# Optimization experiments

Measured on AMD Instinct MI355X. Metric: run time of the kernel, lower is better.

## Reference

```python
import jax, jax.numpy as jnp
import numpy as np

H = 8
DH = 64  # attention_head_size
HID = 512
NEG = -90000000000.0

def _lin(x, w, b):
    return x @ w + b

def _tfs(x):  # [N, HID] -> [H, N, DH]
    n = x.shape[0]
    return x.reshape(n, H, DH).transpose(1, 0, 2)

def _cross(q, ck, v, cv, mask, dw, db):
    # q: [H,N,DH], ck/cv: [H,M,DH], v: [H,N,DH], mask: [N,M]
    s = jnp.einsum('hnd,hmd->hnm', q, ck)
    s = s * mask[None, :, :] / jnp.sqrt(jnp.asarray(DH, s.dtype))
    s = jnp.where(s == 0.0, NEG, s)  # faithful zero->-inf hack
    p = jax.nn.softmax(s, axis=-1)
    ctx = v + jnp.einsum('hnm,hmd->hnd', p, cv)  # residual add of raw value
    n = ctx.shape[1]
    ctx = ctx.transpose(1, 0, 2).reshape(n, H * DH)
    return _lin(ctx, dw, db)

def setup_inputs() -> dict:
    key = jax.random.key(0)
    ks = jax.random.split(key, 24)
    N1, N2, D1 = 4096, 4096, 300
    d = {}
    d['h_head'] = jax.random.normal(ks[0], (N1, D1), jnp.float32)
    d['h_tail'] = jax.random.normal(ks[1], (N2, HID), jnp.float32)
    d['batch_head'] = jnp.sort(jax.random.randint(ks[2], (N1,), 0, 64))
    d['batch_tail'] = jnp.sort(jax.random.randint(ks[3], (N2,), 0, 64))
    def w(k, i, o):
        return jax.random.normal(k, (i, o), jnp.float32) / np.sqrt(i)
    d['map_w'] = w(ks[4], D1, HID); d['map_b'] = jnp.zeros((HID,), jnp.float32)
    names = ['q1', 'k1', 'v1', 'q2', 'k2', 'v2', 'd1', 'd2']
    for i, nm in enumerate(names):
        d[nm + '_w'] = w(ks[5 + i], HID, HID)
        d[nm + '_b'] = jnp.zeros((HID,), jnp.float32)
    return d

def reference(h_head, h_tail, batch_head, batch_tail,
              map_w, map_b,
              q1_w, q1_b, k1_w, k1_b, v1_w, v1_b,
              q2_w, q2_b, k2_w, k2_b, v2_w, v2_b,
              d1_w, d1_b, d2_w, d2_b):
    hh = _lin(h_head, map_w, map_b)  # n_dim1 != n_dim2 -> map
    q_h = _tfs(_lin(hh, q1_w, q1_b))
    k_h = _tfs(_lin(hh, k1_w, k1_b))
    v_h = _tfs(_lin(hh, v1_w, v1_b))
    q_t = _tfs(_lin(h_tail, q2_w, q2_b))
    k_t = _tfs(_lin(h_tail, k2_w, k2_b))
    v_t = _tfs(_lin(h_tail, v2_w, v2_b))
    mask = (batch_head[:, None] == batch_tail[None, :]).astype(jnp.float32)
    out_head = _cross(q_h, k_t, v_h, v_t, mask, d1_w, d1_b)
    out_tail = _cross(q_t, k_h, v_t, v_h, mask.T, d2_w, d2_b)
    return (out_head, out_tail)
```

## Files before the change

kernel.cpp:

```cpp
#include <hip/hip_runtime.h>
#include <hip/hip_bf16.h>
#include <math.h>


typedef __bf16 bf16x8 __attribute__((ext_vector_type(8)));
typedef __bf16 bf16x4 __attribute__((ext_vector_type(4)));
typedef float  f32x4  __attribute__((ext_vector_type(4)));

#define HID 512
#define NTOK 4096

#define AS1(p) ((const __attribute__((address_space(1))) void*)(p))
#define AS3(p) ((__attribute__((address_space(3))) void*)(p))

__device__ __forceinline__ void fold_tile(
    const float* __restrict__ Wf,
    const float* __restrict__ Mw,
    const float* __restrict__ Mb,
    __bf16* __restrict__ F,
    int bx, int by, char* SMEM)
{
    __bf16* As = (__bf16*)SMEM;
    __bf16* Bs = (__bf16*)(SMEM + 8192);

    const int tid  = threadIdx.x;
    const int wave = tid >> 6;
    const int lane = tid & 63;
    const int quad = lane >> 4;
    const int l16  = lane & 15;
    const int wy   = wave >> 1;
    const int wx   = wave & 1;
    const int rowBase = by * 128;
    const int colBase = bx * 128;

    const int s_row = tid >> 2;
    const int s_gc  = (tid & 3) ^ ((s_row >> 1) & 3);
    const int a_j4 = (tid & 7) * 4;
    const int a_n4 = (tid >> 3) * 4;

    float aR[16];
    float4 b0lo, b0hi, b1lo, b1hi;

    auto loadA = [&](int j0) {
        #pragma unroll
        for (int u = 0; u < 4; ++u)
            *(float4*)&aR[u * 4] =
                *(const float4*)&Wf[(size_t)(j0 + a_j4 + u) * 512 + rowBase + a_n4];
    };
    auto loadRow = [&](int k, int jc, float4& lo, float4& hi) {
        if (k < 300) {
            lo = *(const float4*)&Mw[(size_t)k * 512 + jc];
            hi = *(const float4*)&Mw[(size_t)k * 512 + jc + 4];
        } else if (k == 300) {
            lo = *(const float4*)&Mb[jc];
            hi = *(const float4*)&Mb[jc + 4];
        } else {
            lo = float4{0.f, 0.f, 0.f, 0.f};
            hi = float4{0.f, 0.f, 0.f, 0.f};
        }
    };
    auto loadB = [&](int j0) {
        const int jc = j0 + s_gc * 8;
        loadRow(colBase + s_row,      jc, b0lo, b0hi);
        loadRow(colBase + 64 + s_row, jc, b1lo, b1hi);
    };

    f32x4 acc[4][4] = {};

    loadA(0);
    loadB(0);

    for (int i = 0; i < 16; ++i) {
        __syncthreads();
        #pragma unroll
        for (int v = 0; v < 4; ++v) {
            const int r = a_n4 + v;
            const int p = (a_j4 >> 3) ^ ((r >> 1) & 3);
            bf16x4 w;
            w[0] = (__bf16)aR[0 * 4 + v];
            w[1] = (__bf16)aR[1 * 4 + v];
            w[2] = (__bf16)aR[2 * 4 + v];
            w[3] = (__bf16)aR[3 * 4 + v];
            *(bf16x4*)&As[r * 32 + p * 8 + (a_j4 & 7)] = w;
        }
        {
            bf16x8 v0, v1;
            v0[0]=(__bf16)b0lo.x; v0[1]=(__bf16)b0lo.y; v0[2]=(__bf16)b0lo.z; v0[3]=(__bf16)b0lo.w;
            v0[4]=(__bf16)b0hi.x; v0[5]=(__bf16)b0hi.y; v0[6]=(__bf16)b0hi.z; v0[7]=(__bf16)b0hi.w;
            v1[0]=(__bf16)b1lo.x; v1[1]=(__bf16)b1lo.y; v1[2]=(__bf16)b1lo.z; v1[3]=(__bf16)b1lo.w;
            v1[4]=(__bf16)b1hi.x; v1[5]=(__bf16)b1hi.y; v1[6]=(__bf16)b1hi.z; v1[7]=(__bf16)b1hi.w;
            *(bf16x8*)&Bs[tid * 8]        = v0;
            *(bf16x8*)&Bs[2048 + tid * 8] = v1;
        }
        if (i + 1 < 16) { loadA((i + 1) * 32); loadB((i + 1) * 32); }
        __syncthreads();

        bf16x8 ar[4], br[4];
        #pragma unroll
        for (int ii = 0; ii < 4; ++ii) {
            const int ra = wy * 64 + ii * 16 + l16;
            ar[ii] = *(const bf16x8*)&As[ra * 32 + ((quad ^ ((ra >> 1) & 3)) << 3)];
        }
        #pragma unroll
        for (int jj = 0; jj < 4; ++jj) {
            const int rb = wx * 64 + jj * 16 + l16;
            br[jj] = *(const bf16x8*)&Bs[rb * 32 + ((quad ^ ((rb >> 1) & 3)) << 3)];
        }
        #pragma unroll
        for (int ii = 0; ii < 4; ++ii)
            #pragma unroll
            for (int jj = 0; jj < 4; ++jj)
                acc[ii][jj] = __builtin_amdgcn_mfma_f32_16x16x32_bf16(ar[ii], br[jj], acc[ii][jj], 0, 0, 0);
    }

    #pragma unroll
    for (int jj = 0; jj < 4; ++jj) {
        int col = colBase + wx * 64 + jj * 16 + l16;
        if (col < 320) {
            #pragma unroll
            for (int ii = 0; ii < 4; ++ii) {
                #pragma unroll
                for (int r = 0; r < 4; ++r) {
                    int row = rowBase + wy * 64 + ii * 16 + quad * 4 + r;
                    F[(size_t)row * 320 + col] = (__bf16)acc[ii][jj][r];
                }
            }
        }
    }
}

struct PrepArgs {
    const float* h_head; const float* h_tail;
    const int* bh; const int* bt;
    const float* map_w; const float* map_b;
    const float* qkvw[3];
    const float* tsrc[5]; __bf16* tdst[5];
    __bf16* hh_bf; __bf16* ht_bf;
    __bf16* F[3];
    int* ranges;
};

__global__ __launch_bounds__(256) void fused_prep(PrepArgs pa) {
    const int q = blockIdx.x, z = blockIdx.z, tid = threadIdx.x;
    __shared__ __align__(16) char SMEM[16384];

    if (z == 0) {
        if (q == 0 && tid < 128) {
            int b = tid & 63;
            const int* arr = (tid < 64) ? pa.bh : pa.bt;
            int base = (tid < 64) ? 0 : 128;
            int lo = 0, hi = NTOK;
            while (lo < hi) { int mid = (lo + hi) >> 1; if (arr[mid] < b) lo = mid + 1; else hi = mid; }
            int start = lo;
            lo = 0; hi = NTOK;
            while (lo < hi) { int mid = (lo + hi) >> 1; if (arr[mid] <= b) lo = mid + 1; else hi = mid; }
            pa.ranges[base + b] = start;
            pa.ranges[base + 64 + b] = lo;
        }
        for (int idx = tid; idx < 8 * 40; idx += 256) {
            int r   = q * 8 + idx / 40;
            int col = (idx % 40) * 8;
            bf16x8 v;
            if (col + 8 <= 300) {
                float4 f0 = *(const float4*)&pa.h_head[(size_t)r * 300 + col];
                float4 f1 = *(const float4*)&pa.h_head[(size_t)r * 300 + col + 4];
                v[0]=(__bf16)f0.x; v[1]=(__bf16)f0.y; v[2]=(__bf16)f0.z; v[3]=(__bf16)f0.w;
                v[4]=(__bf16)f1.x; v[5]=(__bf16)f1.y; v[6]=(__bf16)f1.z; v[7]=(__bf16)f1.w;
            } else if (col < 300) {
                float4 f0 = *(const float4*)&pa.h_head[(size_t)r * 300 + col];
                v[0]=(__bf16)f0.x; v[1]=(__bf16)f0.y; v[2]=(__bf16)f0.z; v[3]=(__bf16)f0.w;
                v[4]=(__bf16)1.0f;
                v[5]=(__bf16)0.f; v[6]=(__bf16)0.f; v[7]=(__bf16)0.f;
            } else {
                #pragma unroll
                for (int j = 0; j < 8; ++j) v[j] = (__bf16)0.f;
            }
            *(bf16x8*)&pa.hh_bf[(size_t)r * 320 + col] = v;
        }
    } else if (z == 1) {
        for (int idx = tid; idx < 8 * 64; idx += 256) {
            int r   = q * 8 + (idx >> 6);
            int col = (idx & 63) * 8;
            float4 f0 = *(const float4*)&pa.h_tail[(size_t)r * 512 + col];
            float4 f1 = *(const float4*)&pa.h_tail[(size_t)r * 512 + col + 4];
            bf16x8 v;
            v[0]=(__bf16)f0.x; v[1]=(__bf16)f0.y; v[2]=(__bf16)f0.z; v[3]=(__bf16)f0.w;
            v[4]=(__bf16)f1.x; v[5]=(__bf16)f1.y; v[6]=(__bf16)f1.z; v[7]=(__bf16)f1.w;
            *(bf16x8*)&pa.ht_bf[(size_t)r * 512 + col] = v;
        }
    } else if (z == 2) {
        if (q >= 36) return;
        const int f = q / 12, t = q % 12;
        fold_tile(pa.qkvw[f], pa.map_w, pa.map_b, pa.F[f], t % 3, t / 3, SMEM);
    } else {
        if (q >= 64) return;
        typedef __bf16 trow[72];
        trow* T = (trow*)SMEM;
        const int jz = z - 3;
        const float* src = pa.tsrc[jz];
        __bf16* dst = pa.tdst[jz];
        const int tk = (q >> 3) * 64;
        const int tn = (q & 7) * 64;
        const int r0 = tid >> 4;
        const int c0 = (tid & 15) * 4;
        #pragma unroll
        for (int i = 0; i < 4; ++i) {
            float4 v = *(const float4*)&src[(size_t)(tk + r0 + i * 16) * 512 + tn + c0];
            T[r0 + i * 16][c0 + 0] = (__bf16)v.x;
            T[r0 + i * 16][c0 + 1] = (__bf16)v.y;
            T[r0 + i * 16][c0 + 2] = (__bf16)v.z;
            T[r0 + i * 16][c0 + 3] = (__bf16)v.w;
        }
        __syncthreads();
        const int n  = tid >> 2;
        const int kk = (tid & 3) * 16;
        bf16x8 o0, o1;
        #pragma unroll
        for (int j = 0; j < 8; ++j) { o0[j] = T[kk + j][n]; o1[j] = T[kk + 8 + j][n]; }
        __bf16* dp = dst + (size_t)(tn + n) * 512 + tk + kk;
        *(bf16x8*)dp       = o0;
        *(bf16x8*)(dp + 8) = o1;
    }
}

struct GemmJobs {
    const __bf16* A[6];
    const __bf16* W[6];
    const float*  bias[6];
    void*         C[6];
    int           Kp[6];
};

template <typename TC>
__global__ __launch_bounds__(256) void gemm128(GemmJobs jobs) {
    __shared__ __align__(16) __bf16 As[2][4096];
    __shared__ __align__(16) __bf16 Bs[2][4096];

    const int z = blockIdx.z;
    const __bf16* A    = jobs.A[z];
    const __bf16* W    = jobs.W[z];
    const float*  bias = jobs.bias[z];
    TC*           C    = (TC*)jobs.C[z];
    const int     Kp   = jobs.Kp[z];

    const int tid  = threadIdx.x;
    const int wave = tid >> 6;
    const int lane = tid & 63;
    const int quad = lane >> 4;
    const int l16  = lane & 15;
    const int wy   = wave >> 1;
    const int wx   = wave & 1;
    const int rowBase = blockIdx.y * 128;
    const int colBase = blockIdx.x * 128;

    const int s_row = tid >> 2;
    const int s_kc  = ((tid & 3) ^ ((s_row >> 1) & 3)) * 8;

    const __bf16* gA = A + (size_t)(rowBase + s_row) * Kp + s_kc;
    const __bf16* gB = W + (size_t)(colBase + s_row) * Kp + s_kc;
    const int waveOff = wave * 512;

    f32x4 acc[4][4] = {};
    const int nk = Kp >> 5;

    __builtin_amdgcn_global_load_lds(AS1(gA),                   AS3(&As[0][waveOff]),        16, 0, 0);
    __builtin_amdgcn_global_load_lds(AS1(gA + (size_t)64 * Kp), AS3(&As[0][2048 + waveOff]), 16, 0, 0);
    __builtin_amdgcn_global_load_lds(AS1(gB),                   AS3(&Bs[0][waveOff]),        16, 0, 0);
    __builtin_amdgcn_global_load_lds(AS1(gB + (size_t)64 * Kp), AS3(&Bs[0][2048 + waveOff]), 16, 0, 0);

    for (int i = 0; i < nk; ++i) {
        const int cur = i & 1;
        __syncthreads();

        if (i + 1 < nk) {
            const int kt = (i + 1) * 32;
            const int nx = cur ^ 1;
            __builtin_amdgcn_global_load_lds(AS1(gA + kt),                   AS3(&As[nx][waveOff]),        16, 0, 0);
            __builtin_amdgcn_global_load_lds(AS1(gA + kt + (size_t)64 * Kp), AS3(&As[nx][2048 + waveOff]), 16, 0, 0);
            __builtin_amdgcn_global_load_lds(AS1(gB + kt),                   AS3(&Bs[nx][waveOff]),        16, 0, 0);
            __builtin_amdgcn_global_load_lds(AS1(gB + kt + (size_t)64 * Kp), AS3(&Bs[nx][2048 + waveOff]), 16, 0, 0);
        }

        bf16x8 ar[4], br[4];
        #pragma unroll
        for (int ii = 0; ii < 4; ++ii) {
            const int ra = wy * 64 + ii * 16 + l16;
            ar[ii] = *(const bf16x8*)&As[cur][ra * 32 + ((quad ^ ((ra >> 1) & 3)) << 3)];
        }
        #pragma unroll
        for (int jj = 0; jj < 4; ++jj) {
            const int rb = wx * 64 + jj * 16 + l16;
            br[jj] = *(const bf16x8*)&Bs[cur][rb * 32 + ((quad ^ ((rb >> 1) & 3)) << 3)];
        }
        #pragma unroll
        for (int ii = 0; ii < 4; ++ii)
            #pragma unroll
            for (int jj = 0; jj < 4; ++jj)
                acc[ii][jj] = __builtin_amdgcn_mfma_f32_16x16x32_bf16(ar[ii], br[jj], acc[ii][jj], 0, 0, 0);
    }

    #pragma unroll
    for (int jj = 0; jj < 4; ++jj) {
        int col = colBase + wx * 64 + jj * 16 + l16;
        float bv = bias[col];
        #pragma unroll
        for (int ii = 0; ii < 4; ++ii) {
            #pragma unroll
            for (int r = 0; r < 4; ++r) {
                int row = rowBase + wy * 64 + ii * 16 + quad * 4 + r;
                C[(size_t)row * HID + col] = (TC)(acc[ii][jj][r] + bv);
            }
        }
    }
}

__global__ __launch_bounds__(256) void attn_mfma(
    const __bf16* __restrict__ Q0, const __bf16* __restrict__ K0,
    const __bf16* __restrict__ Vr0, const __bf16* __restrict__ Vc0,
    const __bf16* __restrict__ Q1, const __bf16* __restrict__ K1,
    const __bf16* __restrict__ Vr1, const __bf16* __restrict__ Vc1,
    const int* __restrict__ ranges,
    __bf16* __restrict__ O0, __bf16* __restrict__ O1,
    int Nq, int Nk)
{
    __shared__ __align__(16) __bf16 Qs[64][72];
    __shared__ __align__(16) __bf16 Ks[64][72];
    __shared__ __align__(16) __bf16 Vt[64][72];
    __shared__ __align__(16) __bf16 Ps[64][72];

    const int z = blockIdx.z;
    const __bf16* Q    = z ? Q1 : Q0;
    const __bf16* Kg   = z ? K1 : K0;
    const __bf16* Vres = z ? Vr1 : Vr0;
    const __bf16* Vctx = z ? Vc1 : Vc0;
    __bf16* Out        = z ? O1 : O0;
    const int* qstart  = z ? ranges + 128 : ranges;
    const int* qend    = z ? ranges + 192 : ranges + 64;
    const int* kstart  = z ? ranges       : ranges + 128;
    const int* kend    = z ? ranges + 64  : ranges + 192;

    const int h = blockIdx.x, b = blockIdx.y;
    const int qs = qstart[b], qe = qend[b];
    const int ts = kstart[b], te = kend[b];
    const int nq = qe - qs, nk = te - ts;
    if (nq <= 0) return;

    const int tid  = threadIdx.x;
    const int wave = tid >> 6;
    const int lane = tid & 63;
    const int quad = lane >> 4;
    const int l16  = lane & 15;
    const int srow = tid >> 2;
    const int scol = (tid & 3) * 16;

    if (nk <= 0) {
        float* meanv = (float*)Qs;
        if (tid < 64) {
            float s = 0.f;
            for (int m = 0; m < Nk; ++m)
                s += (float)Vctx[(size_t)m * HID + h * 64 + tid];
            meanv[tid] = s / (float)Nk;
        }
        __syncthreads();
        int d = tid & 63;
        for (int r = qs + (tid >> 6); r < qe; r += 4) {
            size_t off = (size_t)r * HID + h * 64 + d;
            Out[off] = (__bf16)((float)Vres[off] + meanv[d]);
        }
        return;
    }

    for (int qc = 0; qc < nq; qc += 64) {
        __syncthreads();
        {
            int qg = min(qs + qc + srow, Nq - 1);
            const __bf16* src = Q + (size_t)qg * HID + h * 64 + scol;
            *(bf16x8*)&Qs[srow][scol]     = *(const bf16x8*)src;
            *(bf16x8*)&Qs[srow][scol + 8] = *(const bf16x8*)(src + 8);
        }
        __syncthreads();
        bf16x8 aq0 = *(const bf16x8*)&Qs[wave * 16 + l16][quad * 8];
        bf16x8 aq1 = *(const bf16x8*)&Qs[wave * 16 + l16][32 + quad * 8];

        f32x4 O[4] = {};
        float Mx[4], L[4];
        #pragma unroll
        for (int r = 0; r < 4; ++r) { Mx[r] = -__builtin_inff(); L[r] = 0.f; }

        for (int kc = 0; kc < nk; kc += 64) {
            __syncthreads();
            {
                int kg = min(ts + kc + srow, Nk - 1);
                const __bf16* ksrc = Kg + (size_t)kg * HID + h * 64 + scol;
                *(bf16x8*)&Ks[srow][scol]     = *(const bf16x8*)ksrc;
                *(bf16x8*)&Ks[srow][scol + 8] = *(const bf16x8*)(ksrc + 8);
                const __bf16* vsrc = Vctx + (size_t)kg * HID + h * 64 + scol;
                bf16x8 v0 = *(const bf16x8*)vsrc;
                bf16x8 v1 = *(const bf16x8*)(vsrc + 8);
                #pragma unroll
                for (int j = 0; j < 8; ++j) {
                    Vt[scol + j][srow]     = v0[j];
                    Vt[scol + 8 + j][srow] = v1[j];
                }
            }
            __syncthreads();

            f32x4 S[4] = {};
            #pragma unroll
            for (int c = 0; c < 4; ++c) {
                bf16x8 bk0 = *(const bf16x8*)&Ks[c * 16 + l16][quad * 8];
                bf16x8 bk1 = *(const bf16x8*)&Ks[c * 16 + l16][32 + quad * 8];
                S[c] = __builtin_amdgcn_mfma_f32_16x16x32_bf16(aq0, bk0, S[c], 0, 0, 0);
                S[c] = __builtin_amdgcn_mfma_f32_16x16x32_bf16(aq1, bk1, S[c], 0, 0, 0);
            }

            #pragma unroll
            for (int c = 0; c < 4; ++c) {
                bool valid = (ts + kc + c * 16 + l16) < te;
                #pragma unroll
                for (int r = 0; r < 4; ++r)
                    S[c][r] = valid ? S[c][r] * 0.125f : -__builtin_inff();
            }

            float cm[4], ps[4], alpha[4];
            #pragma unroll
            for (int r = 0; r < 4; ++r) {
                float v = fmaxf(fmaxf(S[0][r], S[1][r]), fmaxf(S[2][r], S[3][r]));
                v = fmaxf(v, __shfl_xor(v, 1, 64));
                v = fmaxf(v, __shfl_xor(v, 2, 64));
                v = fmaxf(v, __shfl_xor(v, 4, 64));
                v = fmaxf(v, __shfl_xor(v, 8, 64));
                cm[r] = v;
            }
            #pragma unroll
            for (int r = 0; r < 4; ++r) {
                float nM = fmaxf(Mx[r], cm[r]);
                alpha[r] = __expf(Mx[r] - nM);
                Mx[r] = nM;
                ps[r] = 0.f;
            }
            #pragma unroll
            for (int c = 0; c < 4; ++c)
                #pragma unroll
                for (int r = 0; r < 4; ++r) {
                    float p = __expf(S[c][r] - Mx[r]);
                    S[c][r] = p;
                    ps[r] += p;
                }
            #pragma unroll
            for (int r = 0; r < 4; ++r) {
                float v = ps[r];
                v += __shfl_xor(v, 1, 64);
                v += __shfl_xor(v, 2, 64);
                v += __shfl_xor(v, 4, 64);
                v += __shfl_xor(v, 8, 64);
                L[r] = L[r] * alpha[r] + v;
            }
            #pragma unroll
            for (int c = 0; c < 4; ++c)
                #pragma unroll
                for (int r = 0; r < 4; ++r)
                    O[c][r] *= alpha[r];

            #pragma unroll
            for (int c = 0; c < 4; ++c)
                #pragma unroll
                for (int r = 0; r < 4; ++r)
                    Ps[wave * 16 + quad * 4 + r][c * 16 + l16] = (__bf16)S[c][r];
            __syncthreads();

            bf16x8 ap0 = *(const bf16x8*)&Ps[wave * 16 + l16][quad * 8];
            bf16x8 ap1 = *(const bf16x8*)&Ps[wave * 16 + l16][32 + quad * 8];
            #pragma unroll
            for (int c = 0; c < 4; ++c) {
                bf16x8 bv0 = *(const bf16x8*)&Vt[c * 16 + l16][quad * 8];
                bf16x8 bv1 = *(const bf16x8*)&Vt[c * 16 + l16][32 + quad * 8];
                O[c] = __builtin_amdgcn_mfma_f32_16x16x32_bf16(ap0, bv0, O[c], 0, 0, 0);
                O[c] = __builtin_amdgcn_mfma_f32_16x16x32_bf16(ap1, bv1, O[c], 0, 0, 0);
            }
        }

        #pragma unroll
        for (int c = 0; c < 4; ++c) {
            int d = h * 64 + c * 16 + l16;
            #pragma unroll
            for (int r = 0; r < 4; ++r) {
                int qrow = qs + qc + wave * 16 + quad * 4 + r;
                if (qrow < qe) {
                    size_t off = (size_t)qrow * HID + d;
                    Out[off] = (__bf16)((float)Vres[off] + O[c][r] / L[r]);
                }
            }
        }
    }
}

extern "C" void kernel_launch(void* const* d_in, const int* in_sizes, int n_in,
                              void* d_out, int out_size, void* d_ws, size_t ws_size,
                              hipStream_t stream) {
    (void)in_sizes; (void)n_in; (void)out_size; (void)ws_size;

    const float* h_head = (const float*)d_in[0];
    const float* h_tail = (const float*)d_in[1];
    const int* batch_head = (const int*)d_in[2];
    const int* batch_tail = (const int*)d_in[3];
    const float* map_w = (const float*)d_in[4];
    const float* map_b = (const float*)d_in[5];
    const float* q1_w = (const float*)d_in[6];
    const float* q1_b = (const float*)d_in[7];
    const float* k1_w = (const float*)d_in[8];
    const float* k1_b = (const float*)d_in[9];
    const float* v1_w = (const float*)d_in[10];
    const float* v1_b = (const float*)d_in[11];
    const float* q2_w = (const float*)d_in[12];
    const float* q2_b = (const float*)d_in[13];
    const float* k2_w = (const float*)d_in[14];
    const float* k2_b = (const float*)d_in[15];
    const float* v2_w = (const float*)d_in[16];
    const float* v2_b = (const float*)d_in[17];
    const float* d1_w = (const float*)d_in[18];
    const float* d1_b = (const float*)d_in[19];
    const float* d2_w = (const float*)d_in[20];
    const float* d2_b = (const float*)d_in[21];

    float* out = (float*)d_out;

    const size_t SZ = (size_t)NTOK * HID;
    char* ws = (char*)d_ws;
    int* ranges   = (int*)ws;
    __bf16* hh_bf = (__bf16*)(ws + 1024);
    __bf16* ht_bf = hh_bf + (size_t)NTOK * 320;
    __bf16* q2T  = ht_bf + SZ;
    __bf16* k2T  = q2T + 512 * 512;
    __bf16* v2T  = k2T + 512 * 512;
    __bf16* d1T  = v2T + 512 * 512;
    __bf16* d2T  = d1T + 512 * 512;
    __bf16* FqT  = d2T + 512 * 512;
    __bf16* FkT  = FqT + 512 * 320;
    __bf16* FvT  = FkT + 512 * 320;
    __bf16* qh   = FvT + 512 * 320;
    __bf16* kh   = qh  + SZ;
    __bf16* vh   = kh  + SZ;
    __bf16* qt   = vh  + SZ;
    __bf16* kt   = qt  + SZ;
    __bf16* vt   = kt  + SZ;
    __bf16* ctxh = vt  + SZ;
    __bf16* ctxt = ctxh + SZ;

    PrepArgs pa;
    pa.h_head = h_head; pa.h_tail = h_tail;
    pa.bh = batch_head; pa.bt = batch_tail;
    pa.map_w = map_w; pa.map_b = map_b;
    pa.qkvw[0] = q1_w; pa.qkvw[1] = k1_w; pa.qkvw[2] = v1_w;
    const float* wsrc[5] = {q2_w, k2_w, v2_w, d1_w, d2_w};
    __bf16* wdst[5] = {q2T, k2T, v2T, d1T, d2T};
    for (int i = 0; i < 5; ++i) { pa.tsrc[i] = wsrc[i]; pa.tdst[i] = wdst[i]; }
    pa.hh_bf = hh_bf; pa.ht_bf = ht_bf;
    pa.F[0] = FqT; pa.F[1] = FkT; pa.F[2] = FvT;
    pa.ranges = ranges;
    fused_prep<<<dim3(512, 1, 8), dim3(256), 0, stream>>>(pa);

    {
        GemmJobs j;
        j.A[0] = hh_bf; j.W[0] = FqT; j.bias[0] = q1_b; j.C[0] = qh; j.Kp[0] = 320;
        j.A[1] = hh_bf; j.W[1] = FkT; j.bias[1] = k1_b; j.C[1] = kh; j.Kp[1] = 320;
        j.A[2] = hh_bf; j.W[2] = FvT; j.bias[2] = v1_b; j.C[2] = vh; j.Kp[2] = 320;
        j.A[3] = ht_bf; j.W[3] = q2T; j.bias[3] = q2_b; j.C[3] = qt; j.Kp[3] = 512;
        j.A[4] = ht_bf; j.W[4] = k2T; j.bias[4] = k2_b; j.C[4] = kt; j.Kp[4] = 512;
        j.A[5] = ht_bf; j.W[5] = v2T; j.bias[5] = v2_b; j.C[5] = vt; j.Kp[5] = 512;
        gemm128<__bf16><<<dim3(4, 32, 6), dim3(256), 0, stream>>>(j);
    }

    attn_mfma<<<dim3(8, 64, 2), dim3(256), 0, stream>>>(
        qh, kt, vh, vt,
        qt, kh, vt, vh,
        ranges, ctxh, ctxt, NTOK, NTOK);

    {
        GemmJobs j;
        j.A[0] = ctxh; j.W[0] = d1T; j.bias[0] = d1_b; j.C[0] = out;      j.Kp[0] = 512;
        j.A[1] = ctxt; j.W[1] = d2T; j.bias[1] = d2_b; j.C[1] = out + SZ; j.Kp[1] = 512;
        j.A[2] = ctxt; j.W[2] = d2T; j.bias[2] = d2_b; j.C[2] = out + SZ; j.Kp[2] = 512;
        j.A[3] = ctxt; j.W[3] = d2T; j.bias[3] = d2_b; j.C[3] = out + SZ; j.Kp[3] = 512;
        j.A[4] = ctxt; j.W[4] = d2T; j.bias[4] = d2_b; j.C[4] = out + SZ; j.Kp[4] = 512;
        j.A[5] = ctxt; j.W[5] = d2T; j.bias[5] = d2_b; j.C[5] = out + SZ; j.Kp[5] = 512;
        gemm128<float><<<dim3(4, 32, 2), dim3(256), 0, stream>>>(j);
    }
}
```

Before: 184.0 us.

## Read fp32 weights directly in GEMM, drop weight transpose prep stage

```diff
diff --git a/kernel.cpp b/kernel.cpp
--- a/kernel.cpp
+++ b/kernel.cpp
@@ -9,9 +9,6 @@
 
 #define HID 512
 #define NTOK 4096
-
-#define AS1(p) ((const __attribute__((address_space(1))) void*)(p))
-#define AS3(p) ((__attribute__((address_space(3))) void*)(p))
 
 __device__ __forceinline__ void fold_tile(
     const float* __restrict__ Wf,
@@ -134,7 +131,6 @@
     const int* bh; const int* bt;
     const float* map_w; const float* map_b;
     const float* qkvw[3];
-    const float* tsrc[5]; __bf16* tdst[5];
     __bf16* hh_bf; __bf16* ht_bf;
     __bf16* F[3];
     int* ranges;
@@ -188,60 +184,36 @@
             v[4]=(__bf16)f1.x; v[5]=(__bf16)f1.y; v[6]=(__bf16)f1.z; v[7]=(__bf16)f1.w;
             *(bf16x8*)&pa.ht_bf[(size_t)r * 512 + col] = v;
         }
-    } else if (z == 2) {
+    } else {
         if (q >= 36) return;
         const int f = q / 12, t = q % 12;
         fold_tile(pa.qkvw[f], pa.map_w, pa.map_b, pa.F[f], t % 3, t / 3, SMEM);
-    } else {
-        if (q >= 64) return;
-        typedef __bf16 trow[72];
-        trow* T = (trow*)SMEM;
-        const int jz = z - 3;
-        const float* src = pa.tsrc[jz];
-        __bf16* dst = pa.tdst[jz];
-        const int tk = (q >> 3) * 64;
-        const int tn = (q & 7) * 64;
-        const int r0 = tid >> 4;
-        const int c0 = (tid & 15) * 4;
-        #pragma unroll
-        for (int i = 0; i < 4; ++i) {
-            float4 v = *(const float4*)&src[(size_t)(tk + r0 + i * 16) * 512 + tn + c0];
-            T[r0 + i * 16][c0 + 0] = (__bf16)v.x;
-            T[r0 + i * 16][c0 + 1] = (__bf16)v.y;
-            T[r0 + i * 16][c0 + 2] = (__bf16)v.z;
-            T[r0 + i * 16][c0 + 3] = (__bf16)v.w;
-        }
-        __syncthreads();
-        const int n  = tid >> 2;
-        const int kk = (tid & 3) * 16;
-        bf16x8 o0, o1;
-        #pragma unroll
-        for (int j = 0; j < 8; ++j) { o0[j] = T[kk + j][n]; o1[j] = T[kk + 8 + j][n]; }
-        __bf16* dp = dst + (size_t)(tn + n) * 512 + tk + kk;
-        *(bf16x8*)dp       = o0;
-        *(bf16x8*)(dp + 8) = o1;
     }
 }
 
-struct GemmJobs {
-    const __bf16* A[6];
-    const __bf16* W[6];
+struct RSJobs {
+    const __bf16* A[6];   int Ald[6];
+    const void*   B[6];   int Bld[6];  int Bf32t[6];
     const float*  bias[6];
     void*         C[6];
     int           Kp[6];
 };
 
 template <typename TC>
-__global__ __launch_bounds__(256) void gemm128(GemmJobs jobs) {
-    __shared__ __align__(16) __bf16 As[2][4096];
-    __shared__ __align__(16) __bf16 Bs[2][4096];
+__global__ __launch_bounds__(256) void gemm_rs(RSJobs jb) {
+    __shared__ __align__(16) __bf16 As[4096];
+    __shared__ __align__(16) __bf16 Bs[4096];
 
     const int z = blockIdx.z;
-    const __bf16* A    = jobs.A[z];
-    const __bf16* W    = jobs.W[z];
-    const float*  bias = jobs.bias[z];
-    TC*           C    = (TC*)jobs.C[z];
-    const int     Kp   = jobs.Kp[z];
+    const __bf16* A    = jb.A[z];
+    const int     Ald  = jb.Ald[z];
+    const int     f32t = jb.Bf32t[z];
+    const float*  Bf   = (const float*)jb.B[z];
+    const __bf16* Bb   = (const __bf16*)jb.B[z];
+    const int     Bld  = jb.Bld[z];
+    const float*  bias = jb.bias[z];
+    TC*           C    = (TC*)jb.C[z];
+    const int     Kp   = jb.Kp[z];
 
     const int tid  = threadIdx.x;
     const int wave = tid >> 6;
@@ -253,44 +225,71 @@
     const int rowBase = blockIdx.y * 128;
     const int colBase = blockIdx.x * 128;
 
-    const int s_row = tid >> 2;
-    const int s_kc  = ((tid & 3) ^ ((s_row >> 1) & 3)) * 8;
-
-    const __bf16* gA = A + (size_t)(rowBase + s_row) * Kp + s_kc;
-    const __bf16* gB = W + (size_t)(colBase + s_row) * Kp + s_kc;
-    const int waveOff = wave * 512;
+    const int n_row = tid >> 2;
+    const int n_off = ((tid & 3) ^ ((n_row >> 1) & 3)) * 8;
+    const int t_j4 = (tid & 7) * 4;
+    const int t_n4 = (tid >> 3) * 4;
+
+    bf16x8 aR[2];
+    bf16x8 bRb[2];
+    float  bRf[16];
+
+    auto loadT = [&](int k0) {
+        #pragma unroll
+        for (int h = 0; h < 2; ++h)
+            aR[h] = *(const bf16x8*)&A[(size_t)(rowBase + n_row + 64 * h) * Ald + k0 + n_off];
+        if (f32t) {
+            #pragma unroll
+            for (int u = 0; u < 4; ++u)
+                *(float4*)&bRf[u * 4] =
+                    *(const float4*)&Bf[(size_t)(k0 + t_j4 + u) * Bld + colBase + t_n4];
+        } else {
+            #pragma unroll
+            for (int h = 0; h < 2; ++h)
+                bRb[h] = *(const bf16x8*)&Bb[(size_t)(colBase + n_row + 64 * h) * Bld + k0 + n_off];
+        }
+    };
 
     f32x4 acc[4][4] = {};
     const int nk = Kp >> 5;
 
-    __builtin_amdgcn_global_load_lds(AS1(gA),                   AS3(&As[0][waveOff]),        16, 0, 0);
-    __builtin_amdgcn_global_load_lds(AS1(gA + (size_t)64 * Kp), AS3(&As[0][2048 + waveOff]), 16, 0, 0);
-    __builtin_amdgcn_global_load_lds(AS1(gB),                   AS3(&Bs[0][waveOff]),        16, 0, 0);
-    __builtin_amdgcn_global_load_lds(AS1(gB + (size_t)64 * Kp), AS3(&Bs[0][2048 + waveOff]), 16, 0, 0);
+    loadT(0);
 
     for (int i = 0; i < nk; ++i) {
-        const int cur = i & 1;
-        __syncthreads();
-
-        if (i + 1 < nk) {
-            const int kt = (i + 1) * 32;
-            const int nx = cur ^ 1;
-            __builtin_amdgcn_global_load_lds(AS1(gA + kt),                   AS3(&As[nx][waveOff]),        16, 0, 0);
-            __builtin_amdgcn_global_load_lds(AS1(gA + kt + (size_t)64 * Kp), AS3(&As[nx][2048 + waveOff]), 16, 0, 0);
-            __builtin_amdgcn_global_load_lds(AS1(gB + kt),                   AS3(&Bs[nx][waveOff]),        16, 0, 0);
-            __builtin_amdgcn_global_load_lds(AS1(gB + kt + (size_t)64 * Kp), AS3(&Bs[nx][2048 + waveOff]), 16, 0, 0);
-        }
+        __syncthreads();
+        #pragma unroll
+        for (int h = 0; h < 2; ++h)
+            *(bf16x8*)&As[h * 2048 + tid * 8] = aR[h];
+        if (f32t) {
+            #pragma unroll
+            for (int v = 0; v < 4; ++v) {
+                const int r = t_n4 + v;
+                const int p = (t_j4 >> 3) ^ ((r >> 1) & 3);
+                bf16x4 w;
+                w[0] = (__bf16)bRf[0 * 4 + v];
+                w[1] = (__bf16)bRf[1 * 4 + v];
+                w[2] = (__bf16)bRf[2 * 4 + v];
+                w[3] = (__bf16)bRf[3 * 4 + v];
+                *(bf16x4*)&Bs[r * 32 + p * 8 + (t_j4 & 7)] = w;
+            }
+        } else {
+            #pragma unroll
+            for (int h = 0; h < 2; ++h)
+                *(bf16x8*)&Bs[h * 2048 + tid * 8] = bRb[h];
+        }
+        if (i + 1 < nk) loadT((i + 1) * 32);
+        __syncthreads();
 
         bf16x8 ar[4], br[4];
         #pragma unroll
         for (int ii = 0; ii < 4; ++ii) {
             const int ra = wy * 64 + ii * 16 + l16;
-            ar[ii] = *(const bf16x8*)&As[cur][ra * 32 + ((quad ^ ((ra >> 1) & 3)) << 3)];
+            ar[ii] = *(const bf16x8*)&As[ra * 32 + ((quad ^ ((ra >> 1) & 3)) << 3)];
         }
         #pragma unroll
         for (int jj = 0; jj < 4; ++jj) {
             const int rb = wx * 64 + jj * 16 + l16;
-            br[jj] = *(const bf16x8*)&Bs[cur][rb * 32 + ((quad ^ ((rb >> 1) & 3)) << 3)];
+            br[jj] = *(const bf16x8*)&Bs[rb * 32 + ((quad ^ ((rb >> 1) & 3)) << 3)];
         }
         #pragma unroll
         for (int ii = 0; ii < 4; ++ii)
@@ -530,12 +529,7 @@
     int* ranges   = (int*)ws;
     __bf16* hh_bf = (__bf16*)(ws + 1024);
     __bf16* ht_bf = hh_bf + (size_t)NTOK * 320;
-    __bf16* q2T  = ht_bf + SZ;
-    __bf16* k2T  = q2T + 512 * 512;
-    __bf16* v2T  = k2T + 512 * 512;
-    __bf16* d1T  = v2T + 512 * 512;
-    __bf16* d2T  = d1T + 512 * 512;
-    __bf16* FqT  = d2T + 512 * 512;
+    __bf16* FqT  = ht_bf + SZ;
     __bf16* FkT  = FqT + 512 * 320;
     __bf16* FvT  = FkT + 512 * 320;
     __bf16* qh   = FvT + 512 * 320;
@@ -552,23 +546,26 @@
     pa.bh = batch_head; pa.bt = batch_tail;
     pa.map_w = map_w; pa.map_b = map_b;
     pa.qkvw[0] = q1_w; pa.qkvw[1] = k1_w; pa.qkvw[2] = v1_w;
-    const float* wsrc[5] = {q2_w, k2_w, v2_w, d1_w, d2_w};
-    __bf16* wdst[5] = {q2T, k2T, v2T, d1T, d2T};
-    for (int i = 0; i < 5; ++i) { pa.tsrc[i] = wsrc[i]; pa.tdst[i] = wdst[i]; }
     pa.hh_bf = hh_bf; pa.ht_bf = ht_bf;
     pa.F[0] = FqT; pa.F[1] = FkT; pa.F[2] = FvT;
     pa.ranges = ranges;
-    fused_prep<<<dim3(512, 1, 8), dim3(256), 0, stream>>>(pa);
+    fused_prep<<<dim3(512, 1, 3), dim3(256), 0, stream>>>(pa);
 
     {
-        GemmJobs j;
-        j.A[0] = hh_bf; j.W[0] = FqT; j.bias[0] = q1_b; j.C[0] = qh; j.Kp[0] = 320;
-        j.A[1] = hh_bf; j.W[1] = FkT; j.bias[1] = k1_b; j.C[1] = kh; j.Kp[1] = 320;
-        j.A[2] = hh_bf; j.W[2] = FvT; j.bias[2] = v1_b; j.C[2] = vh; j.Kp[2] = 320;
-        j.A[3] = ht_bf; j.W[3] = q2T; j.bias[3] = q2_b; j.C[3] = qt; j.Kp[3] = 512;
-        j.A[4] = ht_bf; j.W[4] = k2T; j.bias[4] = k2_b; j.C[4] = kt; j.Kp[4] = 512;
-        j.A[5] = ht_bf; j.W[5] = v2T; j.bias[5] = v2_b; j.C[5] = vt; j.Kp[5] = 512;
-        gemm128<__bf16><<<dim3(4, 32, 6), dim3(256), 0, stream>>>(j);
+        RSJobs j;
+        j.A[0] = hh_bf; j.Ald[0] = 320; j.B[0] = FqT;  j.Bld[0] = 320; j.Bf32t[0] = 0;
+        j.bias[0] = q1_b; j.C[0] = qh; j.Kp[0] = 320;
+        j.A[1] = hh_bf; j.Ald[1] = 320; j.B[1] = FkT;  j.Bld[1] = 320; j.Bf32t[1] = 0;
+        j.bias[1] = k1_b; j.C[1] = kh; j.Kp[1] = 320;
+        j.A[2] = hh_bf; j.Ald[2] = 320; j.B[2] = FvT;  j.Bld[2] = 320; j.Bf32t[2] = 0;
+        j.bias[2] = v1_b; j.C[2] = vh; j.Kp[2] = 320;
+        j.A[3] = ht_bf; j.Ald[3] = 512; j.B[3] = q2_w; j.Bld[3] = 512; j.Bf32t[3] = 1;
+        j.bias[3] = q2_b; j.C[3] = qt; j.Kp[3] = 512;
+        j.A[4] = ht_bf; j.Ald[4] = 512; j.B[4] = k2_w; j.Bld[4] = 512; j.Bf32t[4] = 1;
+        j.bias[4] = k2_b; j.C[4] = kt; j.Kp[4] = 512;
+        j.A[5] = ht_bf; j.Ald[5] = 512; j.B[5] = v2_w; j.Bld[5] = 512; j.Bf32t[5] = 1;
+        j.bias[5] = v2_b; j.C[5] = vt; j.Kp[5] = 512;
+        gemm_rs<__bf16><<<dim3(4, 32, 6), dim3(256), 0, stream>>>(j);
     }
 
     attn_mfma<<<dim3(8, 64, 2), dim3(256), 0, stream>>>(
@@ -577,13 +574,16 @@
         ranges, ctxh, ctxt, NTOK, NTOK);
 
     {
-        GemmJobs j;
-        j.A[0] = ctxh; j.W[0] = d1T; j.bias[0] = d1_b; j.C[0] = out;      j.Kp[0] = 512;
-        j.A[1] = ctxt; j.W[1] = d2T; j.bias[1] = d2_b; j.C[1] = out + SZ; j.Kp[1] = 512;
-        j.A[2] = ctxt; j.W[2] = d2T; j.bias[2] = d2_b; j.C[2] = out + SZ; j.Kp[2] = 512;
-        j.A[3] = ctxt; j.W[3] = d2T; j.bias[3] = d2_b; j.C[3] = out + SZ; j.Kp[3] = 512;
-        j.A[4] = ctxt; j.W[4] = d2T; j.bias[4] = d2_b; j.C[4] = out + SZ; j.Kp[4] = 512;
-        j.A[5] = ctxt; j.W[5] = d2T; j.bias[5] = d2_b; j.C[5] = out + SZ; j.Kp[5] = 512;
-        gemm128<float><<<dim3(4, 32, 2), dim3(256), 0, stream>>>(j);
+        RSJobs j;
+        for (int i = 0; i < 6; ++i) {
+            int s = (i < 2) ? i : 1;
+            j.A[i] = s ? ctxt : ctxh; j.Ald[i] = 512;
+            j.B[i] = s ? (const void*)d2_w : (const void*)d1_w;
+            j.Bld[i] = 512; j.Bf32t[i] = 1;
+            j.bias[i] = s ? d2_b : d1_b;
+            j.C[i] = s ? (void*)(out + SZ) : (void*)out;
+            j.Kp[i] = 512;
+        }
+        gemm_rs<float><<<dim3(4, 32, 2), dim3(256), 0, stream>>>(j);
     }
 }
```

Result: slower. 193.0 us (+4.9%).
